# Optimization experiments

Hardware: AMD Instinct MI355X
Metric: run time of the kernel (lower is better)

## Reference

```python
import jax, jax.numpy as jnp
import numpy as np

B, C, H, W = 8, 512, 32, 32
NUM_HEADS = 8
NUM_GROUPS = 32
EPS = 1e-5


def setup_inputs() -> dict:
    key = jax.random.key(0)
    k1, k2, k3 = jax.random.split(key, 3)
    x = jax.random.normal(k1, (B, C, H, W), dtype=jnp.float32)
    gn_w = jnp.ones((C,), dtype=jnp.float32)
    gn_b = jnp.zeros((C,), dtype=jnp.float32)
    qkv_w = jax.random.normal(k2, (3 * C, C), dtype=jnp.float32) * 0.02
    qkv_b = jnp.zeros((3 * C,), dtype=jnp.float32)
    # NOTE: original zero-initializes proj_out; we use random weights so the
    # residual branch is non-trivial for correctness testing.
    proj_w = jax.random.normal(k3, (C, C), dtype=jnp.float32) * 0.02
    proj_b = jnp.zeros((C,), dtype=jnp.float32)
    return {"x": x, "gn_w": gn_w, "gn_b": gn_b, "qkv_w": qkv_w,
            "qkv_b": qkv_b, "proj_w": proj_w, "proj_b": proj_b}


def _group_norm(x, w, b):
    # x: [B, C, T]
    Bn, Cn, T = x.shape
    xg = x.reshape(Bn, NUM_GROUPS, Cn // NUM_GROUPS, T)
    mean = xg.mean(axis=(2, 3), keepdims=True)
    var = xg.var(axis=(2, 3), keepdims=True)
    xn = ((xg - mean) * jax.lax.rsqrt(var + EPS)).reshape(Bn, Cn, T)
    return xn * w[None, :, None] + b[None, :, None]


def reference(x, gn_w, gn_b, qkv_w, qkv_b, proj_w, proj_b):
    b, c = x.shape[0], x.shape[1]
    spatial = x.shape[2:]
    xr = x.reshape(b, c, -1)                      # [B, C, T]
    xn = _group_norm(xr, gn_w, gn_b)
    # 1x1 conv1d: [3C, C] x [B, C, T] -> [B, 3C, T]
    qkv = jnp.einsum('oc,bct->bot', qkv_w, xn) + qkv_b[None, :, None]
    T = qkv.shape[-1]
    qkv = qkv.reshape(b * NUM_HEADS, -1, T)       # [B*Nh, 3*ch, T]
    ch = qkv.shape[1] // 3
    q, k, v = jnp.split(qkv, 3, axis=1)
    scale = 1.0 / np.sqrt(np.sqrt(ch))
    weight = jnp.einsum('bct,bcs->bts', q * scale, k * scale)  # [B*Nh, T, T]
    weight = jax.nn.softmax(weight.astype(jnp.float32), axis=-1).astype(weight.dtype)
    h = jnp.einsum('bts,bcs->bct', weight, v)     # [B*Nh, ch, T]
    h = h.reshape(b, c, T)
    h = jnp.einsum('oc,bct->bot', proj_w, h) + proj_b[None, :, None]
    return (xr + h).reshape(b, c, *spatial)
```

## Files before the change

### kernel.cpp

```cpp
#include <hip/hip_runtime.h>
#include <math.h>

#define Bn 8
#define Cn 512
#define Tn 1024

typedef __attribute__((ext_vector_type(8))) short bf16x8;
typedef __attribute__((ext_vector_type(4))) float f32x4;

__device__ __forceinline__ unsigned short f2bf(float f) {
  unsigned int u = __builtin_bit_cast(unsigned int, f);
  u = (u + 0x7FFFu + ((u >> 16) & 1u)) >> 16;
  return (unsigned short)u;
}

typedef __attribute__((address_space(1))) const unsigned int GU32;
typedef __attribute__((address_space(3))) unsigned int LU32;
__device__ __forceinline__ void gld16(const unsigned short* g, unsigned short* l) {
  __builtin_amdgcn_global_load_lds((GU32*)g, (LU32*)l, 16, 0, 0);
}

__device__ __forceinline__ void stage128x64(const unsigned short* __restrict__ src,
                                            size_t row_stride, unsigned short* lds, int tid) {
  const int w = tid >> 6;
  const int row = tid >> 3;
  const int sc = (tid & 7) ^ ((tid >> 3) & 7);
#pragma unroll
  for (int c = 0; c < 4; ++c)
    gld16(src + (size_t)(c * 32 + row) * row_stride + sc * 8,
          (unsigned short*)((char*)lds + c * 4096 + w * 1024));
}

__global__ __launch_bounds__(256) void gn_kernel(const float* __restrict__ x,
                                                 const float* __restrict__ gw,
                                                 const float* __restrict__ gb,
                                                 unsigned short* __restrict__ xn_t) {
  const int blk = blockIdx.x;
  const int b = blk >> 5, g = blk & 31;
  const size_t base = ((size_t)b * Cn + (size_t)g * 16) * Tn;
  const float4* __restrict__ xin = (const float4*)(x + base);
  const int tid = threadIdx.x;

  float vv[16][4];
  float sum = 0.f, sq = 0.f;
#pragma unroll
  for (int k = 0; k < 16; ++k) {
    const float4 t4 = xin[tid + (k << 8)];
    vv[k][0] = t4.x; vv[k][1] = t4.y; vv[k][2] = t4.z; vv[k][3] = t4.w;
    sum += t4.x + t4.y + t4.z + t4.w;
    sq += t4.x * t4.x + t4.y * t4.y + t4.z * t4.z + t4.w * t4.w;
  }

  __shared__ float rs[8];
  const int lane = tid & 63, wv = tid >> 6;
#pragma unroll
  for (int off = 32; off > 0; off >>= 1) {
    sum += __shfl_down(sum, off);
    sq += __shfl_down(sq, off);
  }
  if (lane == 0) { rs[wv] = sum; rs[4 + wv] = sq; }
  __syncthreads();
  const float ts = rs[0] + rs[1] + rs[2] + rs[3];
  const float tq = rs[4] + rs[5] + rs[6] + rs[7];
  const float mean = ts * (1.f / 16384.f);
  const float var = tq * (1.f / 16384.f) - mean * mean;
  const float rstd = rsqrtf(var + 1e-5f);

  float aa[16], bb[16];
#pragma unroll
  for (int k = 0; k < 16; ++k) {
    aa[k] = rstd * gw[g * 16 + k];
    bb[k] = gb[g * 16 + k] - mean * aa[k];
  }

#pragma unroll
  for (int j = 0; j < 4; ++j) {
    const int t = tid * 4 + j;
    unsigned int pk[8];
#pragma unroll
    for (int k2 = 0; k2 < 8; ++k2) {
      const unsigned int lo = f2bf(vv[2 * k2][j] * aa[2 * k2] + bb[2 * k2]);
      const unsigned int hi = f2bf(vv[2 * k2 + 1][j] * aa[2 * k2 + 1] + bb[2 * k2 + 1]);
      pk[k2] = lo | (hi << 16);
    }
    unsigned short* dst = xn_t + ((size_t)(b * Tn + t)) * Cn + g * 16;
    *(uint4*)dst = make_uint4(pk[0], pk[1], pk[2], pk[3]);
    *((uint4*)dst + 1) = make_uint4(pk[4], pk[5], pk[6], pk[7]);
  }
}

__global__ __launch_bounds__(256) void cvt_kernel(const float* __restrict__ src,
                                                  unsigned short* __restrict__ dst, int n4) {
  const int i = blockIdx.x * 256 + threadIdx.x;
  if (i < n4) {
    const float4 f = ((const float4*)src)[i];
    uint2 o;
    o.x = (unsigned int)f2bf(f.x) | ((unsigned int)f2bf(f.y) << 16);
    o.y = (unsigned int)f2bf(f.z) | ((unsigned int)f2bf(f.w) << 16);
    ((uint2*)dst)[i] = o;
  }
}

__global__ __launch_bounds__(256, 2) void qkv_gemm(const unsigned short* __restrict__ Wb,
                                                   const unsigned short* __restrict__ Xb,
                                                   const float* __restrict__ bias,
                                                   unsigned short* __restrict__ q_t,
                                                   unsigned short* __restrict__ k_t,
                                                   unsigned short* __restrict__ v_t) {
  __shared__ unsigned short As[2][8192];
  __shared__ unsigned short Bs[2][8192];
  const int id = blockIdx.x;
  const int b = id & 7;
  const int inner = id >> 3;
  const int bx = inner % 12, by = inner / 12;
  const int o0 = bx * 128, t0 = by * 128;
  const int tid = threadIdx.x, lane = tid & 63, w = tid >> 6;
  const int wr = w >> 1, wc = w & 1;
  const int ln = lane & 15, g16 = lane >> 4;
  const unsigned short* __restrict__ X = Xb + (size_t)b * Tn * Cn;
  const unsigned short* __restrict__ Wt = Wb + (size_t)o0 * 512;
  const unsigned short* __restrict__ Xt = X + (size_t)t0 * 512;

  f32x4 acc[4][4];
#pragma unroll
  for (int mt = 0; mt < 4; ++mt)
#pragma unroll
    for (int nt = 0; nt < 4; ++nt) acc[mt][nt] = (f32x4){0.f, 0.f, 0.f, 0.f};

  stage128x64(Wt, 512, &As[0][0], tid);
  stage128x64(Xt, 512, &Bs[0][0], tid);
  __syncthreads();

  int buf = 0;
  for (int k0 = 0; k0 < 512; k0 += 64) {
    if (k0 + 64 < 512) {
      stage128x64(Wt + k0 + 64, 512, &As[buf ^ 1][0], tid);
      stage128x64(Xt + k0 + 64, 512, &Bs[buf ^ 1][0], tid);
    }
    const char* Ab = (const char*)&As[buf][0];
    const char* Bb = (const char*)&Bs[buf][0];
    bf16x8 af[4][2], bfr[4][2];
#pragma unroll
    for (int mt = 0; mt < 4; ++mt)
#pragma unroll
      for (int kk = 0; kk < 2; ++kk) {
        const int row = wr * 64 + mt * 16 + ln;
        const int c16 = ((kk << 2) | g16) ^ (ln & 7);
        af[mt][kk] = *(const bf16x8*)(Ab + row * 128 + (c16 << 4));
      }
#pragma unroll
    for (int nt = 0; nt < 4; ++nt)
#pragma unroll
      for (int kk = 0; kk < 2; ++kk) {
        const int row = wc * 64 + nt * 16 + ln;
        const int c16 = ((kk << 2) | g16) ^ (ln & 7);
        bfr[nt][kk] = *(const bf16x8*)(Bb + row * 128 + (c16 << 4));
      }
#pragma unroll
    for (int kk = 0; kk < 2; ++kk)
#pragma unroll
      for (int mt = 0; mt < 4; ++mt)
#pragma unroll
        for (int nt = 0; nt < 4; ++nt)
          acc[mt][nt] =
              __builtin_amdgcn_mfma_f32_16x16x32_bf16(af[mt][kk], bfr[nt][kk], acc[mt][nt], 0, 0, 0);
    __syncthreads();
    buf ^= 1;
  }

  const int o_base = o0 + wr * 64, t_base = t0 + wc * 64;
  const int partw = (o_base >> 6) % 3;
  const int bh = b * 8 + o_base / 192;
  unsigned short (*Vlds)[136] = (unsigned short (*)[136])(&As[0][0]);

  if (partw < 2) {
    unsigned short* qk = (partw == 0 ? q_t : k_t) + (size_t)bh * 65536;
    const float sc = (partw == 0) ? 0.125f : 1.0f;
#pragma unroll
    for (int mt = 0; mt < 4; ++mt) {
      const int ob16 = o_base + mt * 16;
      float bv[4];
#pragma unroll
      for (int r = 0; r < 4; ++r) bv[r] = bias[ob16 + g16 * 4 + r];
#pragma unroll
      for (int nt = 0; nt < 4; ++nt) {
        const int t = t_base + nt * 16 + ln;
        const float v0 = (acc[mt][nt][0] + bv[0]) * sc;
        const float v1 = (acc[mt][nt][1] + bv[1]) * sc;
        const float v2 = (acc[mt][nt][2] + bv[2]) * sc;
        const float v3 = (acc[mt][nt][3] + bv[3]) * sc;
        uint2 pk;
        pk.x = (unsigned int)f2bf(v0) | ((unsigned int)f2bf(v1) << 16);
        pk.y = (unsigned int)f2bf(v2) | ((unsigned int)f2bf(v3) << 16);
        *(uint2*)(qk + (size_t)t * 64 + mt * 16 + g16 * 4) = pk;
      }
    }
  } else {
#pragma unroll
    for (int mt = 0; mt < 4; ++mt) {
      float bv[4];
#pragma unroll
      for (int r = 0; r < 4; ++r) bv[r] = bias[o_base + mt * 16 + g16 * 4 + r];
#pragma unroll
      for (int nt = 0; nt < 4; ++nt)
#pragma unroll
        for (int r = 0; r < 4; ++r)
          Vlds[mt * 16 + g16 * 4 + r][wc * 64 + nt * 16 + ln] = f2bf(acc[mt][nt][r] + bv[r]);
    }
  }
  __syncthreads();
  const int bxm = bx % 3;
  if (bxm) {
    const int o_first = o0 + (bxm - 1) * 64;
    unsigned short* vdst = v_t + (size_t)(b * 8 + o_first / 192) * 65536;
    const int c = tid >> 2, tseg = (tid & 3) << 5;
    const unsigned short* src = &Vlds[c][tseg];
    unsigned short* p = vdst + (size_t)c * Tn + t0 + tseg;
    const uint4 d0 = *(const uint4*)(src);
    const uint4 d1 = *(const uint4*)(src + 8);
    const uint4 d2 = *(const uint4*)(src + 16);
    const uint4 d3 = *(const uint4*)(src + 24);
    *(uint4*)(p) = d0;
    *(uint4*)(p + 8) = d1;
    *(uint4*)(p + 16) = d2;
    *(uint4*)(p + 24) = d3;
  }
}

__global__ __launch_bounds__(128, 2) void attn_kernel(const unsigned short* __restrict__ q_t,
                                                      const unsigned short* __restrict__ k_t,
                                                      const unsigned short* __restrict__ v_t,
                                                      unsigned short* __restrict__ h_t) {
  __shared__ unsigned short P_lds[2][32][72];
  const int id = blockIdx.x;
  const int bh = ((id >> 7) << 3) | (id & 7);
  const int tc = (id >> 3) & 15;
  const int tid = threadIdx.x, lane = tid & 63, w = tid >> 6;
  const int t_wave = tc * 64 + w * 32;
  const int ln = lane & 15, g16 = lane >> 4, g8 = g16 * 8;
  const unsigned short* __restrict__ qbase = q_t + (size_t)bh * 65536;
  const unsigned short* __restrict__ kbase = k_t + (size_t)bh * 65536;
  const unsigned short* __restrict__ vbase = v_t + (size_t)bh * 65536;

  bf16x8 qf[2][2];
#pragma unroll
  for (int mt = 0; mt < 2; ++mt)
#pragma unroll
    for (int kb = 0; kb < 2; ++kb)
      qf[mt][kb] = *(const bf16x8*)(qbase + (size_t)(t_wave + mt * 16 + ln) * 64 + kb * 32 + g8);

  f32x4 o_acc[2][4];
  float m_run[2][4], l_run[2][4];
#pragma unroll
  for (int mt = 0; mt < 2; ++mt) {
#pragma unroll
    for (int nc = 0; nc < 4; ++nc) o_acc[mt][nc] = (f32x4){0.f, 0.f, 0.f, 0.f};
#pragma unroll
    for (int r = 0; r < 4; ++r) { m_run[mt][r] = -1e30f; l_run[mt][r] = 0.f; }
  }

  bf16x8 kf[4][2];
#pragma unroll
  for (int ns = 0; ns < 4; ++ns)
#pragma unroll
    for (int kb = 0; kb < 2; ++kb)
      kf[ns][kb] = *(const bf16x8*)(kbase + (size_t)(ns * 16 + ln) * 64 + kb * 32 + g8);

  for (int st = 0; st < 16; ++st) {
    const int s0 = st << 6;
    f32x4 sacc[2][4];
#pragma unroll
    for (int mt = 0; mt < 2; ++mt)
#pragma unroll
      for (int ns = 0; ns < 4; ++ns) sacc[mt][ns] = (f32x4){0.f, 0.f, 0.f, 0.f};

    __builtin_amdgcn_s_setprio(1);
#pragma unroll
    for (int ns = 0; ns < 4; ++ns)
#pragma unroll
      for (int kb = 0; kb < 2; ++kb) {
        sacc[0][ns] = __builtin_amdgcn_mfma_f32_16x16x32_bf16(qf[0][kb], kf[ns][kb], sacc[0][ns], 0, 0, 0);
        sacc[1][ns] = __builtin_amdgcn_mfma_f32_16x16x32_bf16(qf[1][kb], kf[ns][kb], sacc[1][ns], 0, 0, 0);
      }
    __builtin_amdgcn_s_setprio(0);

    bf16x8 vf[4][2];
#pragma unroll
    for (int nc = 0; nc < 4; ++nc)
#pragma unroll
      for (int kb = 0; kb < 2; ++kb)
        vf[nc][kb] = *(const bf16x8*)(vbase + (size_t)(nc * 16 + ln) * Tn + s0 + kb * 32 + g8);

    float mx[2][4];
    bool need = false;
#pragma unroll
    for (int mt = 0; mt < 2; ++mt)
#pragma unroll
      for (int r = 0; r < 4; ++r) {
        float m = fmaxf(fmaxf(sacc[mt][0][r], sacc[mt][1][r]),
                        fmaxf(sacc[mt][2][r], sacc[mt][3][r]));
        m = fmaxf(m, __shfl_xor(m, 1));
        m = fmaxf(m, __shfl_xor(m, 2));
        m = fmaxf(m, __shfl_xor(m, 4));
        m = fmaxf(m, __shfl_xor(m, 8));
        mx[mt][r] = m;
        need = need || (m > m_run[mt][r] + 8.f);
      }
    if (__any(need ? 1 : 0)) {
#pragma unroll
      for (int mt = 0; mt < 2; ++mt)
#pragma unroll
        for (int r = 0; r < 4; ++r) {
          const float mnew = fmaxf(m_run[mt][r], mx[mt][r]);
          const float al = __expf(m_run[mt][r] - mnew);
          m_run[mt][r] = mnew;
          l_run[mt][r] *= al;
#pragma unroll
          for (int nc = 0; nc < 4; ++nc) o_acc[mt][nc][r] *= al;
        }
    }

#pragma unroll
    for (int mt = 0; mt < 2; ++mt)
#pragma unroll
      for (int r = 0; r < 4; ++r) {
        const int trow = mt * 16 + g16 * 4 + r;
        const float mref = m_run[mt][r];
        float rsum = 0.f;
#pragma unroll
        for (int ns = 0; ns < 4; ++ns) {
          const float pv = __expf(sacc[mt][ns][r] - mref);
          rsum += pv;
          P_lds[w][trow][ns * 16 + ln] = f2bf(pv);
        }
        rsum += __shfl_xor(rsum, 1);
        rsum += __shfl_xor(rsum, 2);
        rsum += __shfl_xor(rsum, 4);
        rsum += __shfl_xor(rsum, 8);
        l_run[mt][r] += rsum;
      }

    if (st < 15) {
#pragma unroll
      for (int ns = 0; ns < 4; ++ns)
#pragma unroll
        for (int kb = 0; kb < 2; ++kb)
          kf[ns][kb] =
              *(const bf16x8*)(kbase + (size_t)(s0 + 64 + ns * 16 + ln) * 64 + kb * 32 + g8);
    }

    bf16x8 pf[2][2];
#pragma unroll
    for (int mt = 0; mt < 2; ++mt)
#pragma unroll
      for (int kb = 0; kb < 2; ++kb)
        pf[mt][kb] = *(const bf16x8*)&P_lds[w][mt * 16 + ln][kb * 32 + g8];

    __builtin_amdgcn_s_setprio(1);
#pragma unroll
    for (int kb = 0; kb < 2; ++kb)
#pragma unroll
      for (int nc = 0; nc < 4; ++nc) {
        o_acc[0][nc] = __builtin_amdgcn_mfma_f32_16x16x32_bf16(pf[0][kb], vf[nc][kb], o_acc[0][nc], 0, 0, 0);
        o_acc[1][nc] = __builtin_amdgcn_mfma_f32_16x16x32_bf16(pf[1][kb], vf[nc][kb], o_acc[1][nc], 0, 0, 0);
      }
    __builtin_amdgcn_s_setprio(0);
  }

  const int b = bh >> 3, hh = bh & 7;
  unsigned short* __restrict__ hb = h_t + (size_t)b * Tn * Cn + hh * 64;
#pragma unroll
  for (int mt = 0; mt < 2; ++mt) {
    float rl[4];
#pragma unroll
    for (int r = 0; r < 4; ++r) rl[r] = 1.f / l_run[mt][r];
#pragma unroll
    for (int nc = 0; nc < 4; ++nc) {
      const int c = nc * 16 + ln;
#pragma unroll
      for (int r = 0; r < 4; ++r) {
        const int t = t_wave + mt * 16 + g16 * 4 + r;
        hb[(size_t)t * Cn + c] = f2bf(o_acc[mt][nc][r] * rl[r]);
      }
    }
  }
}

__global__ __launch_bounds__(256, 2) void proj_gemm(const unsigned short* __restrict__ Wb,
                                                    const unsigned short* __restrict__ Hb,
                                                    const float* __restrict__ pbias,
                                                    const float* __restrict__ x,
                                                    float* __restrict__ out) {
  __shared__ unsigned short As[2][8192];
  __shared__ unsigned short Bs[2][8192];
  const int id = blockIdx.x;
  const int b = id & 7;
  const int inner = id >> 3;
  const int bx = inner & 3, by = inner >> 2;
  const int o0 = bx * 128, t0 = by * 128;
  const int tid = threadIdx.x, lane = tid & 63, w = tid >> 6;
  const int wr = w >> 1, wc = w & 1;
  const int ln = lane & 15, g16 = lane >> 4;
  const unsigned short* __restrict__ H = Hb + (size_t)b * Tn * Cn;
  const unsigned short* __restrict__ Wt = Wb + (size_t)o0 * 512;
  const unsigned short* __restrict__ Ht = H + (size_t)t0 * 512;

  f32x4 acc[4][4];
#pragma unroll
  for (int mt = 0; mt < 4; ++mt)
#pragma unroll
    for (int nt = 0; nt < 4; ++nt) acc[mt][nt] = (f32x4){0.f, 0.f, 0.f, 0.f};

  stage128x64(Wt, 512, &As[0][0], tid);
  stage128x64(Ht, 512, &Bs[0][0], tid);
  __syncthreads();

  int buf = 0;
  for (int k0 = 0; k0 < 512; k0 += 64) {
    if (k0 + 64 < 512) {
      stage128x64(Wt + k0 + 64, 512, &As[buf ^ 1][0], tid);
      stage128x64(Ht + k0 + 64, 512, &Bs[buf ^ 1][0], tid);
    }
    const char* Ab = (const char*)&As[buf][0];
    const char* Bb = (const char*)&Bs[buf][0];
    bf16x8 af[4][2], bfr[4][2];
#pragma unroll
    for (int mt = 0; mt < 4; ++mt)
#pragma unroll
      for (int kk = 0; kk < 2; ++kk) {
        const int row = wr * 64 + mt * 16 + ln;
        const int c16 = ((kk << 2) | g16) ^ (ln & 7);
        af[mt][kk] = *(const bf16x8*)(Ab + row * 128 + (c16 << 4));
      }
#pragma unroll
    for (int nt = 0; nt < 4; ++nt)
#pragma unroll
      for (int kk = 0; kk < 2; ++kk) {
        const int row = wc * 64 + nt * 16 + ln;
        const int c16 = ((kk << 2) | g16) ^ (ln & 7);
        bfr[nt][kk] = *(const bf16x8*)(Bb + row * 128 + (c16 << 4));
      }
#pragma unroll
    for (int kk = 0; kk < 2; ++kk)
#pragma unroll
      for (int mt = 0; mt < 4; ++mt)
#pragma unroll
        for (int nt = 0; nt < 4; ++nt)
          acc[mt][nt] =
              __builtin_amdgcn_mfma_f32_16x16x32_bf16(af[mt][kk], bfr[nt][kk], acc[mt][nt], 0, 0, 0);
    __syncthreads();
    buf ^= 1;
  }

  const int o_base = o0 + wr * 64, t_base = t0 + wc * 64;
#pragma unroll
  for (int mt = 0; mt < 4; ++mt) {
    const int ob = o_base + mt * 16 + g16 * 4;
    float pb[4];
#pragma unroll
    for (int r = 0; r < 4; ++r) pb[r] = pbias[ob + r];
#pragma unroll
    for (int nt = 0; nt < 4; ++nt) {
      const int t = t_base + nt * 16 + ln;
#pragma unroll
      for (int r = 0; r < 4; ++r) {
        const size_t idx = (size_t)b * Cn * Tn + (size_t)(ob + r) * Tn + t;
        out[idx] = acc[mt][nt][r] + pb[r] + x[idx];
      }
    }
  }
}

extern "C" void kernel_launch(void* const* d_in, const int* in_sizes, int n_in,
                              void* d_out, int out_size, void* d_ws, size_t ws_size,
                              hipStream_t stream) {
  (void)in_sizes; (void)n_in; (void)out_size; (void)ws_size;
  const float* x = (const float*)d_in[0];
  const float* gn_w = (const float*)d_in[1];
  const float* gn_b = (const float*)d_in[2];
  const float* qkv_w = (const float*)d_in[3];
  const float* qkv_b = (const float*)d_in[4];
  const float* proj_w = (const float*)d_in[5];
  const float* proj_b = (const float*)d_in[6];
  float* out = (float*)d_out;

  unsigned short* wsu = (unsigned short*)d_ws;
  unsigned short* xn_t = wsu;
  unsigned short* wqkv = xn_t + (size_t)4194304;
  unsigned short* wproj = wqkv + (size_t)786432;
  unsigned short* q_t = wproj + (size_t)262144;
  unsigned short* k_t = q_t + (size_t)4194304;
  unsigned short* v_t = k_t + (size_t)4194304;
  unsigned short* h_t = v_t + (size_t)4194304;

  gn_kernel<<<dim3(256), 256, 0, stream>>>(x, gn_w, gn_b, xn_t);
  cvt_kernel<<<dim3(768), 256, 0, stream>>>(qkv_w, wqkv, 196608);
  cvt_kernel<<<dim3(256), 256, 0, stream>>>(proj_w, wproj, 65536);
  qkv_gemm<<<dim3(768), 256, 0, stream>>>(wqkv, xn_t, qkv_b, q_t, k_t, v_t);
  attn_kernel<<<dim3(1024), 128, 0, stream>>>(q_t, k_t, v_t, h_t);
  proj_gemm<<<dim3(256), 256, 0, stream>>>(wproj, h_t, proj_b, x, out);
}
```

Baseline: 188.2 us.

## Restructure attention kernel: 4 waves of 16 rows, transposed S, exp2 softmax

The attention kernel now runs 256 threads with each wave owning 16 query rows instead of 32, raising the occupancy hint and cutting per-wave register pressure. S is computed transposed (K as the A operand), so each lane holds one query row's scores and the row max/sum need only two cross-lane shuffles. Softmax uses exp2 with log2(e) folded into the Q scale in the QKV GEMM epilogue, and P is packed with v_cvt_pk_bf16 into a swizzled LDS layout. K tiles are no longer prefetched one step ahead, which may expose more load latency.

```diff
diff --git a/kernel.cpp b/kernel.cpp
--- a/kernel.cpp
+++ b/kernel.cpp
@@ -12,6 +12,12 @@
   unsigned int u = __builtin_bit_cast(unsigned int, f);
   u = (u + 0x7FFFu + ((u >> 16) & 1u)) >> 16;
   return (unsigned short)u;
+}
+
+__device__ __forceinline__ unsigned int cvtpk_bf16(float lo, float hi) {
+  unsigned int r;
+  asm("v_cvt_pk_bf16_f32 %0, %1, %2" : "=v"(r) : "v"(lo), "v"(hi));
+  return r;
 }
 
 typedef __attribute__((address_space(1))) const unsigned int GU32;
@@ -175,7 +181,7 @@
 
   if (partw < 2) {
     unsigned short* qk = (partw == 0 ? q_t : k_t) + (size_t)bh * 65536;
-    const float sc = (partw == 0) ? 0.125f : 1.0f;
+    const float sc = (partw == 0) ? 0.18033688f : 1.0f;
 #pragma unroll
     for (int mt = 0; mt < 4; ++mt) {
       const int ob16 = o_base + mt * 16;
@@ -227,61 +233,60 @@
   }
 }
 
-__global__ __launch_bounds__(128, 2) void attn_kernel(const unsigned short* __restrict__ q_t,
+__global__ __launch_bounds__(256, 4) void attn_kernel(const unsigned short* __restrict__ q_t,
                                                       const unsigned short* __restrict__ k_t,
                                                       const unsigned short* __restrict__ v_t,
                                                       unsigned short* __restrict__ h_t) {
-  __shared__ unsigned short P_lds[2][32][72];
+  __shared__ __align__(16) unsigned short P_lds[4][1024];
   const int id = blockIdx.x;
-  const int bh = ((id >> 7) << 3) | (id & 7);
-  const int tc = (id >> 3) & 15;
+  const int xcd = id & 7, qq = id >> 3;
+  const int bh = ((qq >> 4) << 3) | xcd;
+  const int tc = qq & 15;
   const int tid = threadIdx.x, lane = tid & 63, w = tid >> 6;
-  const int t_wave = tc * 64 + w * 32;
+  const int t_wave = tc * 64 + w * 16;
   const int ln = lane & 15, g16 = lane >> 4, g8 = g16 * 8;
   const unsigned short* __restrict__ qbase = q_t + (size_t)bh * 65536;
   const unsigned short* __restrict__ kbase = k_t + (size_t)bh * 65536;
   const unsigned short* __restrict__ vbase = v_t + (size_t)bh * 65536;
-
-  bf16x8 qf[2][2];
-#pragma unroll
-  for (int mt = 0; mt < 2; ++mt)
-#pragma unroll
-    for (int kb = 0; kb < 2; ++kb)
-      qf[mt][kb] = *(const bf16x8*)(qbase + (size_t)(t_wave + mt * 16 + ln) * 64 + kb * 32 + g8);
-
-  f32x4 o_acc[2][4];
-  float m_run[2][4], l_run[2][4];
-#pragma unroll
-  for (int mt = 0; mt < 2; ++mt) {
-#pragma unroll
-    for (int nc = 0; nc < 4; ++nc) o_acc[mt][nc] = (f32x4){0.f, 0.f, 0.f, 0.f};
-#pragma unroll
-    for (int r = 0; r < 4; ++r) { m_run[mt][r] = -1e30f; l_run[mt][r] = 0.f; }
-  }
-
-  bf16x8 kf[4][2];
+  char* __restrict__ Pb = (char*)P_lds[w];
+
+  int wr_off[4], rd_off[2];
 #pragma unroll
   for (int ns = 0; ns < 4; ++ns)
-#pragma unroll
-    for (int kb = 0; kb < 2; ++kb)
-      kf[ns][kb] = *(const bf16x8*)(kbase + (size_t)(ns * 16 + ln) * 64 + kb * 32 + g8);
+    wr_off[ns] = ln * 128 + ((((ns << 1) | (g16 >> 1)) ^ (ln & 7)) << 4) + ((g16 & 1) << 3);
+#pragma unroll
+  for (int kb = 0; kb < 2; ++kb)
+    rd_off[kb] = ln * 128 + ((((kb << 2) | g16) ^ (ln & 7)) << 4);
+
+  bf16x8 qf[2];
+#pragma unroll
+  for (int kb = 0; kb < 2; ++kb)
+    qf[kb] = *(const bf16x8*)(qbase + (size_t)(t_wave + ln) * 64 + kb * 32 + g8);
+
+  f32x4 o_acc[4];
+#pragma unroll
+  for (int nc = 0; nc < 4; ++nc) o_acc[nc] = (f32x4){0.f, 0.f, 0.f, 0.f};
+  float m_run = -1e30f, l_run = 0.f;
 
   for (int st = 0; st < 16; ++st) {
     const int s0 = st << 6;
-    f32x4 sacc[2][4];
-#pragma unroll
-    for (int mt = 0; mt < 2; ++mt)
-#pragma unroll
-      for (int ns = 0; ns < 4; ++ns) sacc[mt][ns] = (f32x4){0.f, 0.f, 0.f, 0.f};
+    bf16x8 kf[4][2];
+#pragma unroll
+    for (int ns = 0; ns < 4; ++ns)
+#pragma unroll
+      for (int kb = 0; kb < 2; ++kb)
+        kf[ns][kb] = *(const bf16x8*)(kbase + (size_t)(s0 + ns * 16 + ln) * 64 + kb * 32 + g8);
+
+    f32x4 sacc[4];
+#pragma unroll
+    for (int ns = 0; ns < 4; ++ns) sacc[ns] = (f32x4){0.f, 0.f, 0.f, 0.f};
 
     __builtin_amdgcn_s_setprio(1);
 #pragma unroll
-    for (int ns = 0; ns < 4; ++ns)
-#pragma unroll
-      for (int kb = 0; kb < 2; ++kb) {
-        sacc[0][ns] = __builtin_amdgcn_mfma_f32_16x16x32_bf16(qf[0][kb], kf[ns][kb], sacc[0][ns], 0, 0, 0);
-        sacc[1][ns] = __builtin_amdgcn_mfma_f32_16x16x32_bf16(qf[1][kb], kf[ns][kb], sacc[1][ns], 0, 0, 0);
-      }
+    for (int kb = 0; kb < 2; ++kb)
+#pragma unroll
+      for (int ns = 0; ns < 4; ++ns)
+        sacc[ns] = __builtin_amdgcn_mfma_f32_16x16x32_bf16(kf[ns][kb], qf[kb], sacc[ns], 0, 0, 0);
     __builtin_amdgcn_s_setprio(0);
 
     bf16x8 vf[4][2];
@@ -291,97 +296,74 @@
       for (int kb = 0; kb < 2; ++kb)
         vf[nc][kb] = *(const bf16x8*)(vbase + (size_t)(nc * 16 + ln) * Tn + s0 + kb * 32 + g8);
 
-    float mx[2][4];
-    bool need = false;
-#pragma unroll
-    for (int mt = 0; mt < 2; ++mt)
+    float m = sacc[0][0];
+#pragma unroll
+    for (int ns = 0; ns < 4; ++ns)
+#pragma unroll
+      for (int r = 0; r < 4; ++r) m = fmaxf(m, sacc[ns][r]);
+    m = fmaxf(m, __shfl_xor(m, 16));
+    m = fmaxf(m, __shfl_xor(m, 32));
+
+    if (__any((m > m_run + 11.f) ? 1 : 0)) {
+      const float mnew = fmaxf(m_run, m);
+      const float al = __builtin_amdgcn_exp2f(m_run - mnew);
+      m_run = mnew;
+      l_run *= al;
+      float al4[4];
+#pragma unroll
+      for (int r = 0; r < 4; ++r) al4[r] = __shfl(al, (g16 << 2) + r);
+#pragma unroll
+      for (int nc = 0; nc < 4; ++nc)
+#pragma unroll
+        for (int r = 0; r < 4; ++r) o_acc[nc][r] *= al4[r];
+    }
+
+    float rsum = 0.f;
+#pragma unroll
+    for (int ns = 0; ns < 4; ++ns) {
 #pragma unroll
       for (int r = 0; r < 4; ++r) {
-        float m = fmaxf(fmaxf(sacc[mt][0][r], sacc[mt][1][r]),
-                        fmaxf(sacc[mt][2][r], sacc[mt][3][r]));
-        m = fmaxf(m, __shfl_xor(m, 1));
-        m = fmaxf(m, __shfl_xor(m, 2));
-        m = fmaxf(m, __shfl_xor(m, 4));
-        m = fmaxf(m, __shfl_xor(m, 8));
-        mx[mt][r] = m;
-        need = need || (m > m_run[mt][r] + 8.f);
-      }
-    if (__any(need ? 1 : 0)) {
-#pragma unroll
-      for (int mt = 0; mt < 2; ++mt)
-#pragma unroll
-        for (int r = 0; r < 4; ++r) {
-          const float mnew = fmaxf(m_run[mt][r], mx[mt][r]);
-          const float al = __expf(m_run[mt][r] - mnew);
-          m_run[mt][r] = mnew;
-          l_run[mt][r] *= al;
-#pragma unroll
-          for (int nc = 0; nc < 4; ++nc) o_acc[mt][nc][r] *= al;
-        }
-    }
-
-#pragma unroll
-    for (int mt = 0; mt < 2; ++mt)
-#pragma unroll
-      for (int r = 0; r < 4; ++r) {
-        const int trow = mt * 16 + g16 * 4 + r;
-        const float mref = m_run[mt][r];
-        float rsum = 0.f;
-#pragma unroll
-        for (int ns = 0; ns < 4; ++ns) {
-          const float pv = __expf(sacc[mt][ns][r] - mref);
-          rsum += pv;
-          P_lds[w][trow][ns * 16 + ln] = f2bf(pv);
-        }
-        rsum += __shfl_xor(rsum, 1);
-        rsum += __shfl_xor(rsum, 2);
-        rsum += __shfl_xor(rsum, 4);
-        rsum += __shfl_xor(rsum, 8);
-        l_run[mt][r] += rsum;
-      }
-
-    if (st < 15) {
-#pragma unroll
-      for (int ns = 0; ns < 4; ++ns)
-#pragma unroll
-        for (int kb = 0; kb < 2; ++kb)
-          kf[ns][kb] =
-              *(const bf16x8*)(kbase + (size_t)(s0 + 64 + ns * 16 + ln) * 64 + kb * 32 + g8);
-    }
-
-    bf16x8 pf[2][2];
-#pragma unroll
-    for (int mt = 0; mt < 2; ++mt)
-#pragma unroll
-      for (int kb = 0; kb < 2; ++kb)
-        pf[mt][kb] = *(const bf16x8*)&P_lds[w][mt * 16 + ln][kb * 32 + g8];
+        sacc[ns][r] = __builtin_amdgcn_exp2f(sacc[ns][r] - m_run);
+        rsum += sacc[ns][r];
+      }
+    }
+    rsum += __shfl_xor(rsum, 16);
+    rsum += __shfl_xor(rsum, 32);
+    l_run += rsum;
+
+#pragma unroll
+    for (int ns = 0; ns < 4; ++ns) {
+      uint2 pk2;
+      pk2.x = cvtpk_bf16(sacc[ns][0], sacc[ns][1]);
+      pk2.y = cvtpk_bf16(sacc[ns][2], sacc[ns][3]);
+      *(uint2*)(Pb + wr_off[ns]) = pk2;
+    }
+    bf16x8 pf[2];
+#pragma unroll
+    for (int kb = 0; kb < 2; ++kb) pf[kb] = *(const bf16x8*)(Pb + rd_off[kb]);
 
     __builtin_amdgcn_s_setprio(1);
 #pragma unroll
     for (int kb = 0; kb < 2; ++kb)
 #pragma unroll
-      for (int nc = 0; nc < 4; ++nc) {
-        o_acc[0][nc] = __builtin_amdgcn_mfma_f32_16x16x32_bf16(pf[0][kb], vf[nc][kb], o_acc[0][nc], 0, 0, 0);
-        o_acc[1][nc] = __builtin_amdgcn_mfma_f32_16x16x32_bf16(pf[1][kb], vf[nc][kb], o_acc[1][nc], 0, 0, 0);
-      }
+      for (int nc = 0; nc < 4; ++nc)
+        o_acc[nc] = __builtin_amdgcn_mfma_f32_16x16x32_bf16(pf[kb], vf[nc][kb], o_acc[nc], 0, 0, 0);
     __builtin_amdgcn_s_setprio(0);
   }
 
+  const float rl = 1.f / l_run;
+  float rl4[4];
+#pragma unroll
+  for (int r = 0; r < 4; ++r) rl4[r] = __shfl(rl, (g16 << 2) + r);
   const int b = bh >> 3, hh = bh & 7;
   unsigned short* __restrict__ hb = h_t + (size_t)b * Tn * Cn + hh * 64;
 #pragma unroll
-  for (int mt = 0; mt < 2; ++mt) {
-    float rl[4];
-#pragma unroll
-    for (int r = 0; r < 4; ++r) rl[r] = 1.f / l_run[mt][r];
-#pragma unroll
-    for (int nc = 0; nc < 4; ++nc) {
-      const int c = nc * 16 + ln;
-#pragma unroll
-      for (int r = 0; r < 4; ++r) {
-        const int t = t_wave + mt * 16 + g16 * 4 + r;
-        hb[(size_t)t * Cn + c] = f2bf(o_acc[mt][nc][r] * rl[r]);
-      }
+  for (int nc = 0; nc < 4; ++nc) {
+    const int c = nc * 16 + ln;
+#pragma unroll
+    for (int r = 0; r < 4; ++r) {
+      const int t = t_wave + g16 * 4 + r;
+      hb[(size_t)t * Cn + c] = f2bf(o_acc[nc][r] * rl4[r]);
     }
   }
 }
@@ -497,6 +479,6 @@
   cvt_kernel<<<dim3(768), 256, 0, stream>>>(qkv_w, wqkv, 196608);
   cvt_kernel<<<dim3(256), 256, 0, stream>>>(proj_w, wproj, 65536);
   qkv_gemm<<<dim3(768), 256, 0, stream>>>(wqkv, xn_t, qkv_b, q_t, k_t, v_t);
-  attn_kernel<<<dim3(1024), 128, 0, stream>>>(q_t, k_t, v_t, h_t);
+  attn_kernel<<<dim3(1024), 256, 0, stream>>>(q_t, k_t, v_t, h_t);
   proj_gemm<<<dim3(256), 256, 0, stream>>>(wproj, h_t, proj_b, x, out);
 }
```

After: 239.0 us. 1.27x slower.
